# Kernel tuning notes

Hardware: AMD Instinct MI355X
Metric: run time of the kernel (lower is better)

## Reference

```python
import jax, jax.numpy as jnp
import numpy as np

SIGMA = 1.0   # noise std (unit-variance synthetic input)
P = 11        # patch size p1
K = 16        # number of similar patches k1
WIN = 65      # search window w (odd)
S = 3         # reference-patch stride
ALPHA = 0.5   # n2n alpha


def _unfold(x, ksize, stride):
    # (N,1,H,W) -> (N, ksize*ksize, Ho, Wo); kernel positions row-major (== torch F.unfold for C=1)
    return jax.lax.conv_general_dilated_patches(
        x, (ksize, ksize), (stride, stride), 'VALID',
        dimension_numbers=('NCHW', 'OIHW', 'NCHW'))


def block_matching(x, k, p, w, s):
    N, _, H, W = x.shape
    v = w // 2
    assert (H - p + 1) % s == 1 and (W - p + 1) % s == 1  # no edge-case branches needed
    Href = (H - p) // s + 1
    Wref = (W - p) // s + 1
    x_pad = jnp.pad(x, ((0, 0), (0, 0), (v, v), (v, v)))  # zero pad; invalid candidates masked below
    # |patch|^2 / p^2 at every position of the padded image (== F.avg_pool2d(x**2, p))
    sq = jax.lax.reduce_window(x_pad * x_pad, 0.0, jax.lax.add,
                               (1, 1, p, p), (1, 1, 1, 1), 'VALID') / (p * p)
    norms = _unfold(sq, 2 * v + 1, s)                                  # (N,(2v+1)^2,Href,Wref)
    norms = norms.reshape(N, 2 * v + 1, 2 * v + 1, Href, Wref).transpose(0, 3, 4, 1, 2)
    lw = _unfold(x_pad, 2 * v + p, s) / p                              # (N,(2v+p)^2,Href,Wref)
    lw = lw.reshape(N, 2 * v + p, 2 * v + p, Href, Wref).transpose(0, 3, 4, 1, 2)
    G = N * Href * Wref
    lw = lw.reshape(1, G, 2 * v + p, 2 * v + p)
    ref = lw[0, :, v:-v, v:-v][:, None]                                # (G,1,p,p) reference patches
    sp = jax.lax.conv_general_dilated(
        lw, ref, (1, 1), 'VALID',
        dimension_numbers=('NCHW', 'OIHW', 'NCHW'),
        feature_group_count=G)                                         # (1,G,2v+1,2v+1)
    dist = norms.reshape(1, G, 2 * v + 1, 2 * v + 1) - 2.0 * sp
    dist = dist.reshape(N, Href, Wref, 2 * v + 1, 2 * v + 1)
    # mask candidate patches that fall outside the original image (torch uses NaN padding + topk)
    offs = jnp.arange(-v, v + 1)
    hr = jnp.arange(Href) * s
    wr = jnp.arange(Wref) * s
    row_ok = (hr[:, None] + offs >= 0) & (hr[:, None] + offs <= H - p)  # (Href, 2v+1)
    col_ok = (wr[:, None] + offs >= 0) & (wr[:, None] + offs <= W - p)  # (Wref, 2v+1)
    valid = row_ok[:, None, :, None] & col_ok[None, :, None, :]
    dist = jnp.where(valid[None], dist, jnp.inf)
    dist = dist.at[..., v, v].set(-jnp.inf)                            # reference patch always kept
    dist = dist.reshape(N, Href, Wref, (2 * v + 1) ** 2)
    _, idx = jax.lax.top_k(-dist, k)                                   # k smallest distances
    ind_row = idx // (2 * v + 1) - v
    ind_col = idx % (2 * v + 1) - v
    ind = (ind_row + hr[None, :, None, None]) * (W - p + 1) + (ind_col + wr[None, None, :, None])
    return ind.reshape(N, -1)                                          # (N, Href*Wref*k)


def gather_groups(y, indices, k, p):
    N = y.shape[0]
    uf = _unfold(y, p, 1).reshape(N, p * p, -1)                        # (N, n, (H-p+1)(W-p+1))
    Yg = jnp.take_along_axis(uf, indices[:, None, :], axis=2)          # (N, n, L*k)
    L = indices.shape[1] // k
    return Yg.reshape(N, p * p, L, k).transpose(0, 2, 3, 1)            # (N, L, k, n)


def denoise1(Y, sigma):
    # method='n2n', constraints='affine'
    N, B, k, n = Y.shape
    D = n * sigma ** 2
    E = n * ALPHA ** 2 * sigma ** 2
    Ik = jnp.eye(k, dtype=Y.dtype)
    Q = Y @ jnp.swapaxes(Y, 2, 3) + E * Ik                             # (N,B,k,k), SPD
    Lc = jnp.linalg.cholesky(Q)
    Ikb = jnp.broadcast_to(Ik, Q.shape)
    Z = jax.scipy.linalg.solve_triangular(Lc, Ikb, lower=True)
    Qinv = jax.scipy.linalg.solve_triangular(jnp.swapaxes(Lc, 2, 3), Z, lower=False)
    Qinv1 = jnp.sum(Qinv, axis=3, keepdims=True)
    Qinv2 = jnp.sum(Qinv1, axis=2, keepdims=True)
    theta = Ik - (Qinv - (Qinv1 @ jnp.swapaxes(Qinv1, 2, 3)) / Qinv2) * (D + E)
    theta = jnp.swapaxes(theta, 2, 3)
    X_hat = theta @ Y
    weights = 1.0 / jnp.clip(jnp.sum(theta * theta, axis=3, keepdims=True), 1.0 / k, 1.0)
    return X_hat, weights


def _fold(x, H, W, p):
    # inverse of unfold: sum overlapping p x p patches back onto the image grid
    N, n, _ = x.shape
    Hp, Wp = H - p + 1, W - p + 1
    x = x.reshape(N, p, p, Hp, Wp)
    out = jnp.zeros((N, 1, H, W), x.dtype)
    for a in range(p):
        for b in range(p):
            out = out.at[:, 0, a:a + Hp, b:b + Wp].add(x[:, a, b])
    return out


def aggregate(X_hat, weights, indices, H, W, p):
    N, L, k, n = X_hat.shape
    X = (X_hat * weights).reshape(N, L * k, n).transpose(0, 2, 1)      # (N, n, L*k)
    Wt = jnp.broadcast_to(weights, (N, L, k, n)).reshape(N, L * k, n).transpose(0, 2, 1)
    Lfull = (H - p + 1) * (W - p + 1)
    def scat(vals, idx):
        return jnp.zeros((n, Lfull), vals.dtype).at[:, idx].add(vals)
    X_sum = jax.vmap(scat)(X, indices)
    W_sum = jax.vmap(scat)(Wt, indices)
    return _fold(X_sum, H, W, p) / _fold(W_sum, H, W, p)


def _forward(y):
    N, C, H, W = y.shape
    indices = block_matching(y, K, P, WIN, S)
    Yg = gather_groups(y, indices, K, P)
    X_hat, weights = denoise1(Yg, SIGMA)
    return aggregate(X_hat, weights, indices, H, W, P)


def setup_inputs():
    key = jax.random.key(0)
    y = jax.random.normal(key, (4, 1, 128, 128), dtype=jnp.float32)
    return {"y": y}


def reference(y):
    return _forward(y)
```

## Files before the change

### kernel.cpp

```cpp
#include <hip/hip_runtime.h>
#include <math.h>

#define HH 128
#define WW 128
#define NIMG 4
#define PP 11
#define KSIM 16
#define STRIDE_S 3
#define VRAD 32
#define WINW 65
#define NTASK (WINW*9)
#define HREF 40
#define WREF 40
#define NPOS 118
#define WROWS 75
#define WPITCH 84
#define NGROUP (NIMG*HREF*WREF)
#define EPS_E 30.25f
#define DE_C 151.25f
#define INFD 3.0e38f
#define RTASK 292

#define FOOT 84
#define FPITCH 85
#define SPITCH 88

__global__ __launch_bounds__(256, 5)
void bm_kernel(const float* __restrict__ y, int* __restrict__ inds)
{
    __shared__ float win[WROWS][WPITCH];
    __shared__ float swv[4];
    __shared__ int   swi[4];

    const int blk = blockIdx.x;
    const int n   = blk / (HREF*WREF);
    const int rem = blk % (HREF*WREF);
    const int hr  = (rem / WREF) * STRIDE_S;
    const int wr  = (rem % WREF) * STRIDE_S;
    const float* img = y + n * HH * WW;
    const int tid = threadIdx.x;

    for (int t = tid; t < WROWS * WPITCH; t += 256) {
        int r = t / WPITCH, c = t % WPITCH;
        int gr = hr - VRAD + r, gc = wr - VRAD + c;
        float v = 0.f;
        if (c < WROWS && gr >= 0 && gr < HH && gc >= 0 && gc < WW)
            v = img[gr * WW + gc];
        win[r][c] = v;
    }
    __syncthreads();

    float d[3][8];
#pragma unroll
    for (int s = 0; s < 3; s++)
#pragma unroll
        for (int c = 0; c < 8; c++) d[s][c] = INFD;

#pragma unroll
    for (int s = 0; s < 3; s++) {
        int task = tid + (s << 8);
        if (task < NTASK) {
            int drx = task % WINW;
            int c0  = (task / WINW) * 8;
            int rr  = hr + drx - VRAD;
            bool rowok = (rr >= 0 && rr <= HH - PP);
            if (rowok) {
                float dot[8];
                float colsq[18];
#pragma unroll
                for (int c = 0; c < 8; c++) dot[c] = 0.f;
#pragma unroll
                for (int j2 = 0; j2 < 18; j2++) colsq[j2] = 0.f;
                for (int a = 0; a < PP; a++) {
                    const float4* w4 = reinterpret_cast<const float4*>(&win[drx + a][c0]);
                    float4 A0 = w4[0], A1 = w4[1], A2 = w4[2], A3 = w4[3];
                    float2 A4 = *reinterpret_cast<const float2*>(&win[drx + a][c0 + 16]);
                    float wv[18] = {A0.x,A0.y,A0.z,A0.w, A1.x,A1.y,A1.z,A1.w,
                                    A2.x,A2.y,A2.z,A2.w, A3.x,A3.y,A3.z,A3.w,
                                    A4.x,A4.y};
                    const float4* r4 = reinterpret_cast<const float4*>(&win[VRAD + a][VRAD]);
                    float4 R0 = r4[0], R1 = r4[1];
                    float2 R2 = *reinterpret_cast<const float2*>(&win[VRAD + a][VRAD + 8]);
                    float  R3 = win[VRAD + a][VRAD + 10];
                    float rv[11] = {R0.x,R0.y,R0.z,R0.w, R1.x,R1.y,R1.z,R1.w,
                                    R2.x,R2.y, R3};
#pragma unroll
                    for (int j2 = 0; j2 < 18; j2++) colsq[j2] += wv[j2] * wv[j2];
#pragma unroll
                    for (int b = 0; b < PP; b++) {
#pragma unroll
                        for (int c = 0; c < 8; c++)
                            dot[c] += wv[b + c] * rv[b];
                    }
                }
#pragma unroll
                for (int j2 = 1; j2 < 18; j2++) colsq[j2] += colsq[j2 - 1];
#pragma unroll
                for (int c = 0; c < 8; c++) {
                    int dcx = c0 + c;
                    int cc  = wr + dcx - VRAD;
                    float norm = colsq[c + 10] - (c ? colsq[c - 1] : 0.f);
                    if (dcx < WINW && cc >= 0 && cc <= WW - PP)
                        d[s][c] = norm - 2.f * dot[c];
                }
            }
            if (task == RTASK) d[s][0] = -INFD;
        }
    }

    float lval = INFD; int lidx = 0;
#pragma unroll
    for (int s = 0; s < 3; s++)
#pragma unroll
        for (int c = 0; c < 8; c++)
            if (d[s][c] < lval) { lval = d[s][c]; lidx = (s << 3) | c; }

    for (int sel = 0; sel < KSIM; sel++) {
        float rv = lval;
        int   ri = ((tid + ((lidx >> 3) << 8)) << 3) | (lidx & 7);
#pragma unroll
        for (int off = 32; off > 0; off >>= 1) {
            float ov = __shfl_down(rv, off);
            int   oi = __shfl_down(ri, off);
            if (ov < rv) { rv = ov; ri = oi; }
        }
        if ((tid & 63) == 0) { swv[tid >> 6] = rv; swi[tid >> 6] = ri; }
        __syncthreads();
        float bval = swv[0]; int bidx = swi[0];
#pragma unroll
        for (int w2 = 1; w2 < 4; w2++)
            if (swv[w2] < bval) { bval = swv[w2]; bidx = swi[w2]; }
        if (tid == 0) {
            int task2 = bidx >> 3;
            int drx = task2 % WINW;
            int dcx = (task2 / WINW) * 8 + (bidx & 7);
            inds[blk * KSIM + sel] =
                (hr + drx - VRAD) * NPOS + (wr + dcx - VRAD);
        }
        __syncthreads();
        int otid = (bidx >> 3) & 255;
        if (tid == otid) {
            int code = (((bidx >> 3) >> 8) << 3) | (bidx & 7);
            lval = INFD; lidx = 0;
#pragma unroll
            for (int s = 0; s < 3; s++)
#pragma unroll
                for (int c = 0; c < 8; c++) {
                    if (((s << 3) | c) == code) d[s][c] = INFD;
                    if (d[s][c] < lval) { lval = d[s][c]; lidx = (s << 3) | c; }
                }
        }
    }
}

__global__ __launch_bounds__(512, 1)
void dn_kernel(const float* __restrict__ y, const int* __restrict__ inds,
               float2* __restrict__ nd, int R)
{
    __shared__ float  src[FOOT][SPITCH];
    __shared__ float2 accH[42][FPITCH];
    __shared__ float  Qm[16][16][17];
    __shared__ float  s1[16][16];
    __shared__ float  s2[16];
    __shared__ float  wl[16][16];
    __shared__ short  pr_[16][16], pc_[16][16];

    const int blk = blockIdx.x;
    const int n  = blk / 100;
    const int tr = blk % 100;
    const int ti = tr / 10, tj = tr % 10;
    const int r0 = 12 * ti - VRAD, c0 = 12 * tj - VRAD;
    const int tid = threadIdx.x;
    const float* img = y + n * HH * WW;

    if (tid < 256) {
        int g = tid >> 4, m = tid & 15;
        int gg = n * (HREF * WREF) + (ti * 4 + (g >> 2)) * WREF + (tj * 4 + (g & 3));
        int idx = inds[gg * KSIM + m];
        pr_[g][m] = (short)(idx / NPOS);
        pc_[g][m] = (short)(idx % NPOS);
    }
    for (int t = tid; t < FOOT * FOOT; t += 512) {
        int rr = t / FOOT, cc = t % FOOT;
        int gr = r0 + rr, gc = c0 + cc;
        float vv = 0.f;
        if (gr >= 0 && gr < HH && gc >= 0 && gc < WW) vv = img[gr * WW + gc];
        src[rr][cc] = vv;
    }
    __syncthreads();

    for (int k = 0; k < 5; k++) {
        int task = tid + k * 512;
        if (task < 16 * 136) {
            int g = task / 136, e = task % 136;
            int i = (int)((sqrtf(8.f * (float)e + 1.f) - 1.f) * 0.5f + 1e-4f);
            int j = e - i * (i + 1) / 2;
            int ari = pr_[g][i] - r0, aci = pc_[g][i] - c0;
            int arj = pr_[g][j] - r0, acj = pc_[g][j] - c0;
            float s = (i == j) ? EPS_E : 0.f;
            for (int a = 0; a < PP; a++) {
                const float* Ri = &src[ari + a][aci];
                const float* Rj = &src[arj + a][acj];
#pragma unroll
                for (int b = 0; b < PP; b++) s += Ri[b] * Rj[b];
            }
            Qm[g][i][j] = s;
            Qm[g][j][i] = s;
        }
    }
    __syncthreads();

    const int uu = tid >> 8, ii = (tid >> 4) & 15, jj = tid & 15;
    for (int ks = 0; ks < 16; ks++) {
        float fA[8], rk[8], pv[8], aij[8];
#pragma unroll
        for (int k = 0; k < 8; k++) {
            int g = uu + 2 * k;
            fA[k]  = Qm[g][ii][ks];
            rk[k]  = Qm[g][ks][jj];
            pv[k]  = Qm[g][ks][ks];
            aij[k] = Qm[g][ii][jj];
        }
        __syncthreads();
#pragma unroll
        for (int k = 0; k < 8; k++) {
            int g = uu + 2 * k;
            float inv = 1.f / pv[k];
            float nv;
            if (ii == ks) nv = (jj == ks) ? inv : rk[k] * inv;
            else          nv = (jj == ks) ? -fA[k] * inv : aij[k] - fA[k] * rk[k] * inv;
            Qm[g][ii][jj] = nv;
        }
        __syncthreads();
    }

    if (tid < 256) {
        int g = tid >> 4, a = tid & 15;
        float s = 0.f;
#pragma unroll
        for (int b2 = 0; b2 < 16; b2++) s += Qm[g][a][b2];
        s1[g][a] = s;
    }
    __syncthreads();
    if (tid < 16) {
        float s = 0.f;
#pragma unroll
        for (int a = 0; a < 16; a++) s += s1[tid][a];
        s2[tid] = s;
    }
    __syncthreads();
#pragma unroll
    for (int k = 0; k < 8; k++) {
        int g = uu + 2 * k;
        float t = ((ii == jj) ? 1.f : 0.f)
                - (Qm[g][ii][jj] - s1[g][ii] * s1[g][jj] / s2[g]) * DE_C;
        Qm[g][ii][jj] = t;
    }
    __syncthreads();
    if (tid < 256) {
        int g = tid >> 4, r = tid & 15;
        float s = 0.f;
#pragma unroll
        for (int m2 = 0; m2 < 16; m2++) { float t = Qm[g][m2][r]; s += t * t; }
        s = fminf(fmaxf(s, 1.f / 16.f), 1.f);
        wl[g][r] = 1.f / s;
    }
    __syncthreads();
#pragma unroll
    for (int k = 0; k < 8; k++) {
        int g = uu + 2 * k;
        Qm[g][ii][jj] *= wl[g][jj];
    }
    __syncthreads();

    float2* ndI = nd + ((size_t)(blk & (R - 1)) * NIMG + n) * HH * WW;
#pragma unroll 1
    for (int half = 0; half < 2; half++) {
        const int h0 = half * 42;
        for (int t = tid; t < 42 * FPITCH; t += 512)
            ((float2*)accH)[t] = make_float2(0.f, 0.f);
        __syncthreads();

        for (int it = 0; it < 4; it++) {
            int task = tid + it * 512;
            if (task < 16 * 121) {
                int g = task / 121, px = task % 121;
                int dra = px / 11, dca = px % 11;
                float yv[16];
#pragma unroll
                for (int m = 0; m < 16; m++)
                    yv[m] = src[(int)pr_[g][m] - r0 + dra][(int)pc_[g][m] - c0 + dca];
#pragma unroll
                for (int r = 0; r < 16; r++) {
                    int ar = (int)pr_[g][r] - r0;
                    int hA = ar + dra;
                    if (hA >= h0 && hA < h0 + 42) {
                        float xw = 0.f;
#pragma unroll
                        for (int m = 0; m < 16; m++)
                            xw += Qm[g][m][r] * yv[m];
                        int ac = (int)pc_[g][r] - c0;
                        float* cell = (float*)&accH[hA - h0][ac + dca];
                        __hip_atomic_fetch_add(cell,     xw,
                            __ATOMIC_RELAXED, __HIP_MEMORY_SCOPE_WORKGROUP);
                        __hip_atomic_fetch_add(cell + 1, wl[g][r],
                            __ATOMIC_RELAXED, __HIP_MEMORY_SCOPE_WORKGROUP);
                    }
                }
            }
        }
        __syncthreads();

        for (int t = tid; t < 42 * FOOT; t += 512) {
            int rr = t / FOOT, cc = t % FOOT;
            float2 vv = accH[rr][cc];
            if (vv.y != 0.f) {
                int px = (r0 + h0 + rr) * WW + (c0 + cc);
#if defined(__has_builtin) && __has_builtin(__builtin_amdgcn_global_atomic_fadd_v2f32)
                typedef float v2f __attribute__((ext_vector_type(2)));
                __builtin_amdgcn_global_atomic_fadd_v2f32((v2f*)&ndI[px], (v2f){vv.x, vv.y});
#else
                atomicAdd(&ndI[px].x, vv.x);
                atomicAdd(&ndI[px].y, vv.y);
#endif
            }
        }
        __syncthreads();
    }
}

__global__ __launch_bounds__(256)
void fin_kernel(const float2* __restrict__ nd, float* __restrict__ out, int R)
{
    int t = blockIdx.x * 256 + threadIdx.x;
    if (t < NIMG * HH * WW) {
        float sn = 0.f, sd = 0.f;
        for (int r = 0; r < R; r++) {
            float2 vv = nd[(size_t)r * NIMG * HH * WW + t];
            sn += vv.x; sd += vv.y;
        }
        out[t] = sn / sd;
    }
}

extern "C" void kernel_launch(void* const* d_in, const int* in_sizes, int n_in,
                              void* d_out, int out_size, void* d_ws, size_t ws_size,
                              hipStream_t stream)
{
    const float* y = (const float*)d_in[0];
    float* out = (float*)d_out;

    size_t perRep = (size_t)NIMG * HH * WW * sizeof(float2);
    size_t indsB  = (size_t)NGROUP * KSIM * sizeof(int);
    int R = 1;
    while (R < 4 && perRep * (size_t)(R * 2) + indsB <= ws_size) R <<= 1;

    float2* nd   = (float2*)d_ws;
    int*    inds = (int*)((char*)d_ws + perRep * (size_t)R);

    hipMemsetAsync(nd, 0, perRep * (size_t)R, stream);
    bm_kernel<<<NGROUP, 256, 0, stream>>>(y, inds);
    dn_kernel<<<NIMG * 100, 512, 0, stream>>>(y, inds, nd, R);
    fin_kernel<<<(NIMG * HH * WW + 255) / 256, 256, 0, stream>>>(nd, out, R);
}
```

Before: 446.6 us.

## Split denoise into a per-group solve kernel and a tile scatter kernel

The monolithic denoise kernel is split in two. A new solve kernel computes each group's Gram matrix, inverse and weights, with four groups per 256-thread block, and stores the symmetric filter plus weights to workspace. A scatter kernel per tile then reads those, forms the weighted filter rows per thread and accumulates into a single 84x84 shared tile instead of two halves. The aim is more parallelism for the solve phase, which previously ran as only 400 blocks of 512 threads with one block per CU. The costs are an extra launch, a workspace round trip for the filters, and patch values read from global memory instead of shared memory.

```diff
diff --git a/kernel.cpp b/kernel.cpp
--- a/kernel.cpp
+++ b/kernel.cpp
@@ -20,10 +20,7 @@
 #define DE_C 151.25f
 #define INFD 3.0e38f
 #define RTASK 292
-
-#define FOOT 84
-#define FPITCH 85
-#define SPITCH 88
+#define THREC 152
 
 __global__ __launch_bounds__(256, 5)
 void bm_kernel(const float* __restrict__ y, int* __restrict__ inds)
@@ -153,16 +150,124 @@
     }
 }
 
+__global__ __launch_bounds__(256)
+void dn_solve(const float* __restrict__ y, const int* __restrict__ inds,
+              float* __restrict__ thW)
+{
+    __shared__ float Qs[4][16][17];
+    __shared__ float s1[4][16];
+    __shared__ float s2[4];
+    __shared__ float wl[4][16];
+    __shared__ short pr_[4][16], pc_[4][16];
+
+    const int blk = blockIdx.x;
+    const int tid = threadIdx.x;
+    const int g0 = blk * 4;
+
+    if (tid < 64) {
+        int gq = tid >> 4, m = tid & 15;
+        int idx = inds[(g0 + gq) * KSIM + m];
+        pr_[gq][m] = (short)(idx / NPOS);
+        pc_[gq][m] = (short)(idx % NPOS);
+    }
+    __syncthreads();
+
+    for (int t = tid; t < 4 * 136; t += 256) {
+        int gq = t / 136, e = t % 136;
+        int i = (int)((sqrtf(8.f * (float)e + 1.f) - 1.f) * 0.5f + 1e-4f);
+        int j = e - i * (i + 1) / 2;
+        const float* img = y + ((g0 + gq) / (HREF * WREF)) * HH * WW;
+        const float* Pi = img + (int)pr_[gq][i] * WW + (int)pc_[gq][i];
+        const float* Pj = img + (int)pr_[gq][j] * WW + (int)pc_[gq][j];
+        float s = (i == j) ? EPS_E : 0.f;
+        for (int a = 0; a < PP; a++) {
+            const float* Ri = Pi + a * WW;
+            const float* Rj = Pj + a * WW;
+#pragma unroll
+            for (int b = 0; b < PP; b++) s += Ri[b] * Rj[b];
+        }
+        Qs[gq][i][j] = s;
+        Qs[gq][j][i] = s;
+    }
+    __syncthreads();
+
+    const int gq = tid >> 6, ii = (tid >> 2) & 15, jq = tid & 3;
+    for (int ks = 0; ks < 16; ks++) {
+        float fA = Qs[gq][ii][ks];
+        float pv = Qs[gq][ks][ks];
+        float rk[4], aij[4];
+#pragma unroll
+        for (int q = 0; q < 4; q++) {
+            rk[q]  = Qs[gq][ks][jq * 4 + q];
+            aij[q] = Qs[gq][ii][jq * 4 + q];
+        }
+        __syncthreads();
+        float inv = 1.f / pv;
+#pragma unroll
+        for (int q = 0; q < 4; q++) {
+            int jj = jq * 4 + q;
+            float nv;
+            if (ii == ks) nv = (jj == ks) ? inv : rk[q] * inv;
+            else          nv = (jj == ks) ? -fA * inv : aij[q] - fA * rk[q] * inv;
+            Qs[gq][ii][jj] = nv;
+        }
+        __syncthreads();
+    }
+
+    if (jq == 0) {
+        float s = 0.f;
+#pragma unroll
+        for (int b = 0; b < 16; b++) s += Qs[gq][ii][b];
+        s1[gq][ii] = s;
+    }
+    __syncthreads();
+    if (ii == 0 && jq == 0) {
+        float s = 0.f;
+#pragma unroll
+        for (int a = 0; a < 16; a++) s += s1[gq][a];
+        s2[gq] = s;
+    }
+    __syncthreads();
+    {
+        float s1i = s1[gq][ii];
+#pragma unroll
+        for (int q = 0; q < 4; q++) {
+            int jj = jq * 4 + q;
+            float t2 = ((ii == jj) ? 1.f : 0.f)
+                     - (Qs[gq][ii][jj] - s1i * s1[gq][jj] / s2[gq]) * DE_C;
+            Qs[gq][ii][jj] = t2;
+        }
+    }
+    __syncthreads();
+    if (jq == 1) {
+        float s = 0.f;
+#pragma unroll
+        for (int m = 0; m < 16; m++) { float t2 = Qs[gq][m][ii]; s += t2 * t2; }
+        s = fminf(fmaxf(s, 1.f / 16.f), 1.f);
+        wl[gq][ii] = 1.f / s;
+    }
+    __syncthreads();
+
+    for (int t = tid; t < 4 * THREC; t += 256) {
+        int gg = t / THREC, e = t % THREC;
+        float v;
+        if (e < 136) {
+            int i = (int)((sqrtf(8.f * (float)e + 1.f) - 1.f) * 0.5f + 1e-4f);
+            int j = e - i * (i + 1) / 2;
+            v = Qs[gg][i][j];
+        } else {
+            v = wl[gg][e - 136];
+        }
+        thW[(size_t)(g0 + gg) * THREC + e] = v;
+    }
+}
+
 __global__ __launch_bounds__(512, 1)
-void dn_kernel(const float* __restrict__ y, const int* __restrict__ inds,
-               float2* __restrict__ nd, int R)
-{
-    __shared__ float  src[FOOT][SPITCH];
-    __shared__ float2 accH[42][FPITCH];
-    __shared__ float  Qm[16][16][17];
-    __shared__ float  s1[16][16];
-    __shared__ float  s2[16];
-    __shared__ float  wl[16][16];
+void dn_scatter(const float* __restrict__ y, const int* __restrict__ inds,
+                const float* __restrict__ thW, float2* __restrict__ nd, int R)
+{
+    __shared__ float2 acc[84][85];
+    __shared__ float  thS[16][THREC];
     __shared__ short  pr_[16][16], pc_[16][16];
 
     const int blk = blockIdx.x;
@@ -180,152 +285,73 @@
         pr_[g][m] = (short)(idx / NPOS);
         pc_[g][m] = (short)(idx % NPOS);
     }
-    for (int t = tid; t < FOOT * FOOT; t += 512) {
-        int rr = t / FOOT, cc = t % FOOT;
-        int gr = r0 + rr, gc = c0 + cc;
-        float vv = 0.f;
-        if (gr >= 0 && gr < HH && gc >= 0 && gc < WW) vv = img[gr * WW + gc];
-        src[rr][cc] = vv;
-    }
-    __syncthreads();
-
-    for (int k = 0; k < 5; k++) {
-        int task = tid + k * 512;
-        if (task < 16 * 136) {
-            int g = task / 136, e = task % 136;
-            int i = (int)((sqrtf(8.f * (float)e + 1.f) - 1.f) * 0.5f + 1e-4f);
-            int j = e - i * (i + 1) / 2;
-            int ari = pr_[g][i] - r0, aci = pc_[g][i] - c0;
-            int arj = pr_[g][j] - r0, acj = pc_[g][j] - c0;
-            float s = (i == j) ? EPS_E : 0.f;
-            for (int a = 0; a < PP; a++) {
-                const float* Ri = &src[ari + a][aci];
-                const float* Rj = &src[arj + a][acj];
-#pragma unroll
-                for (int b = 0; b < PP; b++) s += Ri[b] * Rj[b];
+    for (int t = tid; t < 16 * THREC; t += 512) {
+        int g = t / THREC, e = t % THREC;
+        int gg = n * (HREF * WREF) + (ti * 4 + (g >> 2)) * WREF + (tj * 4 + (g & 3));
+        thS[g][e] = thW[(size_t)gg * THREC + e];
+    }
+    for (int t = tid; t < 84 * 85; t += 512)
+        ((float2*)acc)[t] = make_float2(0.f, 0.f);
+    __syncthreads();
+
+    const int g6 = tid >> 5, sub = tid & 31, rq = sub >> 2, pq = sub & 3;
+    int bs[16];
+#pragma unroll
+    for (int m = 0; m < 16; m++)
+        bs[m] = (int)pr_[g6][m] * WW + (int)pc_[g6][m];
+    float Ar[2][16]; float wr2[2]; int ar2[2], ac2[2];
+#pragma unroll
+    for (int k = 0; k < 2; k++) {
+        int r = rq * 2 + k;
+        float w = thS[g6][136 + r];
+#pragma unroll
+        for (int m = 0; m < 16; m++) {
+            int hi = (m > r) ? m : r, lo = (m > r) ? r : m;
+            Ar[k][m] = thS[g6][hi * (hi + 1) / 2 + lo] * w;
+        }
+        wr2[k] = w;
+        ar2[k] = (int)pr_[g6][r] - r0;
+        ac2[k] = (int)pc_[g6][r] - c0;
+    }
+
+#pragma unroll 1
+    for (int t = 0; t < 31; t++) {
+        int px = pq * 31 + t;
+        if (px < 121) {
+            int dra = px / 11, dca = px % 11;
+            const int off = dra * WW + dca;
+            float yv[16];
+#pragma unroll
+            for (int m = 0; m < 16; m++) yv[m] = img[bs[m] + off];
+#pragma unroll
+            for (int k = 0; k < 2; k++) {
+                float xw = 0.f;
+#pragma unroll
+                for (int m = 0; m < 16; m++) xw += Ar[k][m] * yv[m];
+                float* cell = (float*)&acc[ar2[k] + dra][ac2[k] + dca];
+                __hip_atomic_fetch_add(cell,     xw,
+                    __ATOMIC_RELAXED, __HIP_MEMORY_SCOPE_WORKGROUP);
+                __hip_atomic_fetch_add(cell + 1, wr2[k],
+                    __ATOMIC_RELAXED, __HIP_MEMORY_SCOPE_WORKGROUP);
             }
-            Qm[g][i][j] = s;
-            Qm[g][j][i] = s;
-        }
-    }
-    __syncthreads();
-
-    const int uu = tid >> 8, ii = (tid >> 4) & 15, jj = tid & 15;
-    for (int ks = 0; ks < 16; ks++) {
-        float fA[8], rk[8], pv[8], aij[8];
-#pragma unroll
-        for (int k = 0; k < 8; k++) {
-            int g = uu + 2 * k;
-            fA[k]  = Qm[g][ii][ks];
-            rk[k]  = Qm[g][ks][jj];
-            pv[k]  = Qm[g][ks][ks];
-            aij[k] = Qm[g][ii][jj];
-        }
-        __syncthreads();
-#pragma unroll
-        for (int k = 0; k < 8; k++) {
-            int g = uu + 2 * k;
-            float inv = 1.f / pv[k];
-            float nv;
-            if (ii == ks) nv = (jj == ks) ? inv : rk[k] * inv;
-            else          nv = (jj == ks) ? -fA[k] * inv : aij[k] - fA[k] * rk[k] * inv;
-            Qm[g][ii][jj] = nv;
-        }
-        __syncthreads();
-    }
-
-    if (tid < 256) {
-        int g = tid >> 4, a = tid & 15;
-        float s = 0.f;
-#pragma unroll
-        for (int b2 = 0; b2 < 16; b2++) s += Qm[g][a][b2];
-        s1[g][a] = s;
-    }
-    __syncthreads();
-    if (tid < 16) {
-        float s = 0.f;
-#pragma unroll
-        for (int a = 0; a < 16; a++) s += s1[tid][a];
-        s2[tid] = s;
-    }
-    __syncthreads();
-#pragma unroll
-    for (int k = 0; k < 8; k++) {
-        int g = uu + 2 * k;
-        float t = ((ii == jj) ? 1.f : 0.f)
-                - (Qm[g][ii][jj] - s1[g][ii] * s1[g][jj] / s2[g]) * DE_C;
-        Qm[g][ii][jj] = t;
-    }
-    __syncthreads();
-    if (tid < 256) {
-        int g = tid >> 4, r = tid & 15;
-        float s = 0.f;
-#pragma unroll
-        for (int m2 = 0; m2 < 16; m2++) { float t = Qm[g][m2][r]; s += t * t; }
-        s = fminf(fmaxf(s, 1.f / 16.f), 1.f);
-        wl[g][r] = 1.f / s;
-    }
-    __syncthreads();
-#pragma unroll
-    for (int k = 0; k < 8; k++) {
-        int g = uu + 2 * k;
-        Qm[g][ii][jj] *= wl[g][jj];
+        }
     }
     __syncthreads();
 
     float2* ndI = nd + ((size_t)(blk & (R - 1)) * NIMG + n) * HH * WW;
-#pragma unroll 1
-    for (int half = 0; half < 2; half++) {
-        const int h0 = half * 42;
-        for (int t = tid; t < 42 * FPITCH; t += 512)
-            ((float2*)accH)[t] = make_float2(0.f, 0.f);
-        __syncthreads();
-
-        for (int it = 0; it < 4; it++) {
-            int task = tid + it * 512;
-            if (task < 16 * 121) {
-                int g = task / 121, px = task % 121;
-                int dra = px / 11, dca = px % 11;
-                float yv[16];
-#pragma unroll
-                for (int m = 0; m < 16; m++)
-                    yv[m] = src[(int)pr_[g][m] - r0 + dra][(int)pc_[g][m] - c0 + dca];
-#pragma unroll
-                for (int r = 0; r < 16; r++) {
-                    int ar = (int)pr_[g][r] - r0;
-                    int hA = ar + dra;
-                    if (hA >= h0 && hA < h0 + 42) {
-                        float xw = 0.f;
-#pragma unroll
-                        for (int m = 0; m < 16; m++)
-                            xw += Qm[g][m][r] * yv[m];
-                        int ac = (int)pc_[g][r] - c0;
-                        float* cell = (float*)&accH[hA - h0][ac + dca];
-                        __hip_atomic_fetch_add(cell,     xw,
-                            __ATOMIC_RELAXED, __HIP_MEMORY_SCOPE_WORKGROUP);
-                        __hip_atomic_fetch_add(cell + 1, wl[g][r],
-                            __ATOMIC_RELAXED, __HIP_MEMORY_SCOPE_WORKGROUP);
-                    }
-                }
-            }
-        }
-        __syncthreads();
-
-        for (int t = tid; t < 42 * FOOT; t += 512) {
-            int rr = t / FOOT, cc = t % FOOT;
-            float2 vv = accH[rr][cc];
-            if (vv.y != 0.f) {
-                int px = (r0 + h0 + rr) * WW + (c0 + cc);
+    for (int t = tid; t < 84 * 84; t += 512) {
+        int rr = t / 84, cc = t % 84;
+        float2 vv = acc[rr][cc];
+        if (vv.y != 0.f) {
+            int px = (r0 + rr) * WW + (c0 + cc);
 #if defined(__has_builtin) && __has_builtin(__builtin_amdgcn_global_atomic_fadd_v2f32)
-                typedef float v2f __attribute__((ext_vector_type(2)));
-                __builtin_amdgcn_global_atomic_fadd_v2f32((v2f*)&ndI[px], (v2f){vv.x, vv.y});
+            typedef float v2f __attribute__((ext_vector_type(2)));
+            __builtin_amdgcn_global_atomic_fadd_v2f32((v2f*)&ndI[px], (v2f){vv.x, vv.y});
 #else
-                atomicAdd(&ndI[px].x, vv.x);
-                atomicAdd(&ndI[px].y, vv.y);
+            atomicAdd(&ndI[px].x, vv.x);
+            atomicAdd(&ndI[px].y, vv.y);
 #endif
-            }
-        }
-        __syncthreads();
+        }
     }
 }
 
@@ -352,14 +378,17 @@
 
     size_t perRep = (size_t)NIMG * HH * WW * sizeof(float2);
     size_t indsB  = (size_t)NGROUP * KSIM * sizeof(int);
+    size_t thWB   = (size_t)NGROUP * THREC * sizeof(float);
     int R = 1;
-    while (R < 4 && perRep * (size_t)(R * 2) + indsB <= ws_size) R <<= 1;
+    while (R < 4 && perRep * (size_t)(R * 2) + indsB + thWB <= ws_size) R <<= 1;
 
     float2* nd   = (float2*)d_ws;
     int*    inds = (int*)((char*)d_ws + perRep * (size_t)R);
+    float*  thW  = (float*)((char*)inds + indsB);
 
     hipMemsetAsync(nd, 0, perRep * (size_t)R, stream);
     bm_kernel<<<NGROUP, 256, 0, stream>>>(y, inds);
-    dn_kernel<<<NIMG * 100, 512, 0, stream>>>(y, inds, nd, R);
+    dn_solve<<<NGROUP / 4, 256, 0, stream>>>(y, inds, thW);
+    dn_scatter<<<NIMG * 100, 512, 0, stream>>>(y, inds, thW, nd, R);
     fin_kernel<<<(NIMG * HH * WW + 255) / 256, 256, 0, stream>>>(nd, out, R);
 }
```

Result: no change. 445.3 us (-0.3%).
